# Kernel optimization log

Hardware: AMD Instinct MI355X
Metric: run time of the kernel (lower is better)

The kernel has to match this reference:

```python
import jax, jax.numpy as jnp
import numpy as np

IN_F = 4096
OUT_F = 4096
THRESH = 0.1

def setup_inputs() -> dict:
    key = jax.random.key(0)
    kx, kw = jax.random.split(key)
    x = jax.random.normal(kx, (4, 2048, IN_F), dtype=jnp.float32)
    weight = jax.random.normal(kw, (OUT_F, IN_F), dtype=jnp.float32) * 0.5
    bias = jnp.zeros((OUT_F,), dtype=jnp.float32)
    return {"x": x, "weight": weight, "bias": bias}

def reference(x, weight, bias):
    # ternary quantization: sign(w) where |w| > 0.1, else 0
    q = jnp.sign(weight) * (jnp.abs(weight) > THRESH).astype(weight.dtype)
    # straight-through estimator: forward uses q, gradient flows to weight
    w_ste = weight + jax.lax.stop_gradient(q - weight)
    # F.linear: x @ w_ste.T + bias
    return jnp.einsum('bsi,oi->bso', x, w_ste) + bias
```

## Files before the change

kernel.cpp:

```cpp
#include <hip/hip_runtime.h>
#include <cstdint>
#include <cstddef>

#define MDIM 8192
#define NDIM 4096
#define KDIM 4096
#define TERN_THRESH 0.1f

typedef unsigned short u16;
typedef __bf16 bf16x8 __attribute__((ext_vector_type(8)));
typedef float f32x4 __attribute__((ext_vector_type(4)));
typedef u16 u16x8 __attribute__((ext_vector_type(8)));


__device__ __forceinline__ u16 f2bf(float f) {
  unsigned u = __float_as_uint(f);
  u += 0x7FFFu + ((u >> 16) & 1u);
  return (u16)(u >> 16);
}

__device__ __forceinline__ u16 tern_bf16(float w) {
  return w > TERN_THRESH ? (u16)0x3F80u : (w < -TERN_THRESH ? (u16)0xBF80u : (u16)0u);
}

__device__ __forceinline__ void load_lds16(const u16* g, u16* s) {
  __builtin_amdgcn_global_load_lds(
      (__attribute__((address_space(1))) void*)(void*)(g),
      (__attribute__((address_space(3))) void*)(void*)(s),
      16, 0, 0);
}


#define XBLOCKS ((MDIM * (size_t)KDIM) / (8 * 256))
#define WBLOCKS ((NDIM * (size_t)KDIM) / (8 * 256))

__global__ __launch_bounds__(256) void cvt_kernel(const float* __restrict__ x,
                                                  u16* __restrict__ xb,
                                                  const float* __restrict__ w,
                                                  u16* __restrict__ qb) {
  size_t b = blockIdx.x;
  if (b < XBLOCKS) {
    size_t i = b * 256 + threadIdx.x;
    const f32x4* x4 = (const f32x4*)x;
    f32x4 a = __builtin_nontemporal_load(&x4[2 * i]);
    f32x4 c = __builtin_nontemporal_load(&x4[2 * i + 1]);
    u16x8 o;
    o[0] = f2bf(a[0]); o[1] = f2bf(a[1]); o[2] = f2bf(a[2]); o[3] = f2bf(a[3]);
    o[4] = f2bf(c[0]); o[5] = f2bf(c[1]); o[6] = f2bf(c[2]); o[7] = f2bf(c[3]);
    ((u16x8*)xb)[i] = o;
  } else {
    size_t i = (b - XBLOCKS) * 256 + threadIdx.x;
    const f32x4* w4 = (const f32x4*)w;
    f32x4 a = __builtin_nontemporal_load(&w4[2 * i]);
    f32x4 c = __builtin_nontemporal_load(&w4[2 * i + 1]);
    u16x8 o;
    o[0] = tern_bf16(a[0]); o[1] = tern_bf16(a[1]); o[2] = tern_bf16(a[2]); o[3] = tern_bf16(a[3]);
    o[4] = tern_bf16(c[0]); o[5] = tern_bf16(c[1]); o[6] = tern_bf16(c[2]); o[7] = tern_bf16(c[3]);
    ((u16x8*)qb)[i] = o;
  }
}


#define NT (KDIM / 64)

#define BARRIER() __builtin_amdgcn_s_barrier()
#define FENCE()   asm volatile("" ::: "memory")
#define VMCNT4()  asm volatile("s_waitcnt vmcnt(4)" ::: "memory")

#define MFMA_BLK(I0)                                                         \
  do {                                                                       \
    _Pragma("unroll") for (int _i = 0; _i < 4; ++_i) {                       \
      _Pragma("unroll") for (int _j = 0; _j < 4; ++_j) {                     \
        acc[(I0) + _i][_j] = __builtin_amdgcn_mfma_f32_16x16x32_bf16(        \
            af[_i], bf[_j], acc[(I0) + _i][_j], 0, 0, 0);                    \
      }                                                                      \
    }                                                                        \
  } while (0)

__global__ __launch_bounds__(512, 2) void gemm_tern_kernel(
    const u16* __restrict__ Xb,
    const u16* __restrict__ Qb,
    const float* __restrict__ bias,
    float* __restrict__ C) {
  __shared__ __attribute__((aligned(16))) u16 As[4 * 8192];
  __shared__ __attribute__((aligned(16))) u16 Bs[4 * 8192];

  const int tid  = threadIdx.x;
  const int lane = tid & 63;
  const int wv   = tid >> 6;
  const int wm   = wv >> 2;
  const int wn   = wv & 3;
  const int quad = lane >> 4;
  const int l16  = lane & 15;

  const int orig    = blockIdx.y * 16 + blockIdx.x;
  const int wg      = (orig & 7) * 64 + (orig >> 3);
  const int rowBase = (wg >> 4) * 256;
  const int colBase = (wg & 15) * 256;

  const u16* gA[2];
  const u16* gB[2];
  int sOff[2];
#pragma unroll
  for (int j = 0; j < 2; ++j) {
    int c  = j * 512 + tid;
    int r  = c >> 2;
    int qg = (c & 3) ^ ((r >> 1) & 3);
    gA[j]   = Xb + (size_t)(rowBase + r) * KDIM + qg * 8;
    gB[j]   = Qb + (size_t)(colBase + r) * KDIM + qg * 8;
    sOff[j] = c * 8;
  }

#define STAGE_A(b, h, ko)                                                        \
  do {                                                                           \
    load_lds16(gA[0] + (ko) + (h) * 32, (u16*)As + ((b) * 2 + (h)) * 8192 + sOff[0]); \
    load_lds16(gA[1] + (ko) + (h) * 32, (u16*)As + ((b) * 2 + (h)) * 8192 + sOff[1]); \
  } while (0)
#define STAGE_B(b, h, ko)                                                        \
  do {                                                                           \
    load_lds16(gB[0] + (ko) + (h) * 32, (u16*)Bs + ((b) * 2 + (h)) * 8192 + sOff[0]); \
    load_lds16(gB[1] + (ko) + (h) * 32, (u16*)Bs + ((b) * 2 + (h)) * 8192 + sOff[1]); \
  } while (0)

  int ac[8], bc[4];
#pragma unroll
  for (int i = 0; i < 8; ++i) {
    int r = wm * 128 + i * 16 + l16;
    ac[i] = (r * 4 + (quad ^ ((r >> 1) & 3))) * 8;
  }
#pragma unroll
  for (int j = 0; j < 4; ++j) {
    int r = wn * 64 + j * 16 + l16;
    bc[j] = (r * 4 + (quad ^ ((r >> 1) & 3))) * 8;
  }

#define RD_A(d, i, b, kk) d = *(const bf16x8*)((const u16*)As + ((b) * 2 + (kk)) * 8192 + ac[i])
#define RD_B(d, j, b, kk) d = *(const bf16x8*)((const u16*)Bs + ((b) * 2 + (kk)) * 8192 + bc[j])

  f32x4 acc[8][4] = {};
  bf16x8 af[4], bf[4];

  STAGE_A(0, 0, 0);
  STAGE_B(0, 0, 0);
  STAGE_A(0, 1, 0);
  STAGE_B(0, 1, 0);
  VMCNT4();
  BARRIER();
  FENCE();

  int cur = 0;
  for (int t = 0; t < NT; ++t) {
    const int nxt = cur ^ 1;
    const int kn  = (t + 1 < NT) ? (t + 1) * 64 : 0;

    RD_A(af[0], 0, cur, 0); RD_A(af[1], 1, cur, 0);
    RD_A(af[2], 2, cur, 0); RD_A(af[3], 3, cur, 0);
    RD_B(bf[0], 0, cur, 0); RD_B(bf[1], 1, cur, 0);
    RD_B(bf[2], 2, cur, 0); RD_B(bf[3], 3, cur, 0);
    STAGE_A(nxt, 0, kn);
    BARRIER(); FENCE();
    __builtin_amdgcn_s_setprio(1);
    MFMA_BLK(0);
    __builtin_amdgcn_s_setprio(0);
    BARRIER(); FENCE();

    RD_A(af[0], 4, cur, 0); RD_A(af[1], 5, cur, 0);
    RD_A(af[2], 6, cur, 0); RD_A(af[3], 7, cur, 0);
    STAGE_B(nxt, 0, kn);
    BARRIER(); FENCE();
    __builtin_amdgcn_s_setprio(1);
    MFMA_BLK(4);
    __builtin_amdgcn_s_setprio(0);
    VMCNT4();
    BARRIER(); FENCE();

    RD_A(af[0], 0, cur, 1); RD_A(af[1], 1, cur, 1);
    RD_A(af[2], 2, cur, 1); RD_A(af[3], 3, cur, 1);
    RD_B(bf[0], 0, cur, 1); RD_B(bf[1], 1, cur, 1);
    RD_B(bf[2], 2, cur, 1); RD_B(bf[3], 3, cur, 1);
    STAGE_A(nxt, 1, kn);
    BARRIER(); FENCE();
    __builtin_amdgcn_s_setprio(1);
    MFMA_BLK(0);
    __builtin_amdgcn_s_setprio(0);
    BARRIER(); FENCE();

    RD_A(af[0], 4, cur, 1); RD_A(af[1], 5, cur, 1);
    RD_A(af[2], 6, cur, 1); RD_A(af[3], 7, cur, 1);
    STAGE_B(nxt, 1, kn);
    BARRIER(); FENCE();
    __builtin_amdgcn_s_setprio(1);
    MFMA_BLK(4);
    __builtin_amdgcn_s_setprio(0);
    VMCNT4();
    BARRIER(); FENCE();

    cur = nxt;
  }

  float bv[4];
#pragma unroll
  for (int j = 0; j < 4; ++j) bv[j] = bias[colBase + wn * 64 + j * 16 + l16];

#pragma unroll
  for (int i = 0; i < 8; ++i) {
#pragma unroll
    for (int r = 0; r < 4; ++r) {
      int grow = rowBase + wm * 128 + i * 16 + quad * 4 + r;
      float* crow = C + (size_t)grow * NDIM + colBase + wn * 64 + l16;
#pragma unroll
      for (int j = 0; j < 4; ++j) {
        crow[j * 16] = acc[i][j][r] + bv[j];
      }
    }
  }
}


extern "C" void kernel_launch(void* const* d_in, const int* in_sizes, int n_in,
                              void* d_out, int out_size, void* d_ws, size_t ws_size,
                              hipStream_t stream) {
  const float* x    = (const float*)d_in[0];
  const float* w    = (const float*)d_in[1];
  const float* bias = (const float*)d_in[2];
  float* out = (float*)d_out;

  u16* xb = (u16*)d_ws;
  u16* qb = xb + (size_t)MDIM * KDIM;

  cvt_kernel<<<(unsigned)(XBLOCKS + WBLOCKS), 256, 0, stream>>>(x, xb, w, qb);

  dim3 grid(NDIM / 256, MDIM / 256);
  gemm_tern_kernel<<<grid, 512, 0, stream>>>(xb, qb, bias, out);
}
```

Baseline: 497.6 us.

## Switch GEMM mainloop to 4-stage ring buffer with 3-tile prefetch depth

Replaces the double-buffered 64-wide K tile scheme (two 32-wide halves per buffer) with a four-slot ring of 32-wide K tiles, prefetching three tiles ahead. The wait count rises from vmcnt(4) to vmcnt(8), and the loop is unrolled by four so slot indices are compile-time constants. The goal is more global-to-LDS loads in flight to hide memory latency behind MFMA work. LDS usage is unchanged. It adds more outstanding loads, and barriers per K element stay the same.

```diff
diff --git a/kernel.cpp b/kernel.cpp
--- a/kernel.cpp
+++ b/kernel.cpp
@@ -61,11 +61,11 @@
 }
 
 
-#define NT (KDIM / 64)
+#define NTILE (KDIM / 32)
 
 #define BARRIER() __builtin_amdgcn_s_barrier()
 #define FENCE()   asm volatile("" ::: "memory")
-#define VMCNT4()  asm volatile("s_waitcnt vmcnt(4)" ::: "memory")
+#define VMCNT8()  asm volatile("s_waitcnt vmcnt(8)" ::: "memory")
 
 #define MFMA_BLK(I0)                                                         \
   do {                                                                       \
@@ -111,15 +111,15 @@
     sOff[j] = c * 8;
   }
 
-#define STAGE_A(b, h, ko)                                                        \
-  do {                                                                           \
-    load_lds16(gA[0] + (ko) + (h) * 32, (u16*)As + ((b) * 2 + (h)) * 8192 + sOff[0]); \
-    load_lds16(gA[1] + (ko) + (h) * 32, (u16*)As + ((b) * 2 + (h)) * 8192 + sOff[1]); \
-  } while (0)
-#define STAGE_B(b, h, ko)                                                        \
-  do {                                                                           \
-    load_lds16(gB[0] + (ko) + (h) * 32, (u16*)Bs + ((b) * 2 + (h)) * 8192 + sOff[0]); \
-    load_lds16(gB[1] + (ko) + (h) * 32, (u16*)Bs + ((b) * 2 + (h)) * 8192 + sOff[1]); \
+#define STAGE_A(s, kt)                                              \
+  do {                                                              \
+    load_lds16(gA[0] + (kt), (u16*)As + (s) * 8192 + sOff[0]);      \
+    load_lds16(gA[1] + (kt), (u16*)As + (s) * 8192 + sOff[1]);      \
+  } while (0)
+#define STAGE_B(s, kt)                                              \
+  do {                                                              \
+    load_lds16(gB[0] + (kt), (u16*)Bs + (s) * 8192 + sOff[0]);      \
+    load_lds16(gB[1] + (kt), (u16*)Bs + (s) * 8192 + sOff[1]);      \
   } while (0)
 
   int ac[8], bc[4];
@@ -134,68 +134,50 @@
     bc[j] = (r * 4 + (quad ^ ((r >> 1) & 3))) * 8;
   }
 
-#define RD_A(d, i, b, kk) d = *(const bf16x8*)((const u16*)As + ((b) * 2 + (kk)) * 8192 + ac[i])
-#define RD_B(d, j, b, kk) d = *(const bf16x8*)((const u16*)Bs + ((b) * 2 + (kk)) * 8192 + bc[j])
+#define RD_A(d, i, s) d = *(const bf16x8*)((const u16*)As + (s) * 8192 + ac[i])
+#define RD_B(d, j, s) d = *(const bf16x8*)((const u16*)Bs + (s) * 8192 + bc[j])
 
   f32x4 acc[8][4] = {};
   bf16x8 af[4], bf[4];
 
-  STAGE_A(0, 0, 0);
-  STAGE_B(0, 0, 0);
-  STAGE_A(0, 1, 0);
-  STAGE_B(0, 1, 0);
-  VMCNT4();
-  BARRIER();
-  FENCE();
-
-  int cur = 0;
-  for (int t = 0; t < NT; ++t) {
-    const int nxt = cur ^ 1;
-    const int kn  = (t + 1 < NT) ? (t + 1) * 64 : 0;
-
-    RD_A(af[0], 0, cur, 0); RD_A(af[1], 1, cur, 0);
-    RD_A(af[2], 2, cur, 0); RD_A(af[3], 3, cur, 0);
-    RD_B(bf[0], 0, cur, 0); RD_B(bf[1], 1, cur, 0);
-    RD_B(bf[2], 2, cur, 0); RD_B(bf[3], 3, cur, 0);
-    STAGE_A(nxt, 0, kn);
-    BARRIER(); FENCE();
-    __builtin_amdgcn_s_setprio(1);
-    MFMA_BLK(0);
-    __builtin_amdgcn_s_setprio(0);
-    BARRIER(); FENCE();
-
-    RD_A(af[0], 4, cur, 0); RD_A(af[1], 5, cur, 0);
-    RD_A(af[2], 6, cur, 0); RD_A(af[3], 7, cur, 0);
-    STAGE_B(nxt, 0, kn);
-    BARRIER(); FENCE();
-    __builtin_amdgcn_s_setprio(1);
-    MFMA_BLK(4);
-    __builtin_amdgcn_s_setprio(0);
-    VMCNT4();
-    BARRIER(); FENCE();
-
-    RD_A(af[0], 0, cur, 1); RD_A(af[1], 1, cur, 1);
-    RD_A(af[2], 2, cur, 1); RD_A(af[3], 3, cur, 1);
-    RD_B(bf[0], 0, cur, 1); RD_B(bf[1], 1, cur, 1);
-    RD_B(bf[2], 2, cur, 1); RD_B(bf[3], 3, cur, 1);
-    STAGE_A(nxt, 1, kn);
-    BARRIER(); FENCE();
-    __builtin_amdgcn_s_setprio(1);
-    MFMA_BLK(0);
-    __builtin_amdgcn_s_setprio(0);
-    BARRIER(); FENCE();
-
-    RD_A(af[0], 4, cur, 1); RD_A(af[1], 5, cur, 1);
-    RD_A(af[2], 6, cur, 1); RD_A(af[3], 7, cur, 1);
-    STAGE_B(nxt, 1, kn);
-    BARRIER(); FENCE();
-    __builtin_amdgcn_s_setprio(1);
-    MFMA_BLK(4);
-    __builtin_amdgcn_s_setprio(0);
-    VMCNT4();
-    BARRIER(); FENCE();
-
-    cur = nxt;
+  STAGE_A(0, 0);  STAGE_B(0, 0);
+  STAGE_A(1, 32); STAGE_B(1, 32);
+  STAGE_A(2, 64); STAGE_B(2, 64);
+  VMCNT8();
+  FENCE(); BARRIER(); FENCE();
+
+#define TILE_BODY(S)                                                       \
+  do {                                                                     \
+    const int kt = (t + 3 < NTILE) ? (t + 3) * 32 : 0;                     \
+                                         \
+    RD_A(af[0], 0, S); RD_A(af[1], 1, S);                                  \
+    RD_A(af[2], 2, S); RD_A(af[3], 3, S);                                  \
+    RD_B(bf[0], 0, S); RD_B(bf[1], 1, S);                                  \
+    RD_B(bf[2], 2, S); RD_B(bf[3], 3, S);                                  \
+    STAGE_A(((S) + 3) & 3, kt);                                            \
+    FENCE(); BARRIER(); FENCE();                                           \
+    __builtin_amdgcn_s_setprio(1);                                         \
+    MFMA_BLK(0);                                                           \
+    __builtin_amdgcn_s_setprio(0);                                         \
+    FENCE(); BARRIER(); FENCE();                                           \
+                                         \
+    RD_A(af[0], 4, S); RD_A(af[1], 5, S);                                  \
+    RD_A(af[2], 6, S); RD_A(af[3], 7, S);                                  \
+    STAGE_B(((S) + 3) & 3, kt);                                            \
+    FENCE(); BARRIER(); FENCE();                                           \
+    __builtin_amdgcn_s_setprio(1);                                         \
+    MFMA_BLK(4);                                                           \
+    __builtin_amdgcn_s_setprio(0);                                         \
+    VMCNT8();                                                              \
+    FENCE(); BARRIER(); FENCE();                                           \
+  } while (0)
+
+  int t = 0;
+  for (int it = 0; it < NTILE / 4; ++it) {
+    TILE_BODY(0); ++t;
+    TILE_BODY(1); ++t;
+    TILE_BODY(2); ++t;
+    TILE_BODY(3); ++t;
   }
 
   float bv[4];
```

Measured after the change: 457.0 us. 1.09x faster.
